# Kernel optimization log

Hardware: AMD Instinct MI355X
Metric: run time of the kernel (lower is better)

## Reference

```python
import jax, jax.numpy as jnp
import numpy as np

N_NODES = 50000
BN_EPS = 1e-5


def graph_conv(x, row, col, ew, n):
    # deg from source indices only (matches torch.bincount(row))
    deg = jnp.zeros((n,), x.dtype).at[row].add(1.0)
    dinv = jnp.where(deg > 0, deg ** -0.5, 0.0)
    norm = dinv[row] * ew * dinv[col]                     # [E]
    msg = norm[:, None] * x[row]                          # [E, F]
    return jax.ops.segment_sum(msg, col, num_segments=n)  # out[dst] += w * x[src]


def batch_norm(x, gamma, beta):
    # training-mode BN over the node (batch) dim, biased variance
    mu = jnp.mean(x, axis=0)
    var = jnp.mean((x - mu) ** 2, axis=0)
    return (x - mu) / jnp.sqrt(var + BN_EPS) * gamma + beta


def setup_inputs() -> dict:
    key = jax.random.key(0)
    ks = jax.random.split(key, 12)
    node_features = jax.random.normal(ks[0], (N_NODES, 100), dtype=jnp.float32)
    edge_index = jax.random.randint(ks[1], (2, 800000), 0, N_NODES, dtype=jnp.int64)
    edge_weights = jax.random.uniform(ks[2], (800000,), dtype=jnp.float32)
    def lin(k, fi, fo):
        lim = 1.0 / np.sqrt(fi)
        k1, k2 = jax.random.split(k)
        W = jax.random.uniform(k1, (fi, fo), minval=-lim, maxval=lim, dtype=jnp.float32)
        b = jax.random.uniform(k2, (fo,), minval=-lim, maxval=lim, dtype=jnp.float32)
        return W, b
    W0, b0 = lin(ks[3], 100, 128)
    W1, b1 = lin(ks[4], 128, 128)
    W2, b2 = lin(ks[5], 128, 64)
    return {
        "node_features": node_features, "edge_index": edge_index, "edge_weights": edge_weights,
        "W0": W0, "b0": b0, "g0": jnp.ones((128,), jnp.float32), "be0": jnp.zeros((128,), jnp.float32),
        "W1": W1, "b1": b1, "g1": jnp.ones((128,), jnp.float32), "be1": jnp.zeros((128,), jnp.float32),
        "W2": W2, "b2": b2,
    }


def reference(node_features, edge_index, edge_weights,
              W0, b0, g0, be0, W1, b1, g1, be1, W2, b2):
    n = node_features.shape[0]
    row, col = edge_index[0], edge_index[1]
    x = node_features
    # layer 0
    x = graph_conv(x, row, col, edge_weights, n)
    x = jax.nn.relu(batch_norm(x @ W0 + b0, g0, be0))
    # layer 1
    x = graph_conv(x, row, col, edge_weights, n)
    x = jax.nn.relu(batch_norm(x @ W1 + b1, g1, be1))
    # final layer (no BN/relu)
    x = graph_conv(x, row, col, edge_weights, n)
    return x @ W2 + b2
```

## Files before the change

### kernel.cpp

```cpp
#include <hip/hip_runtime.h>
#include <cstdint>

#define F0 100
#define FH 128
#define FO 64
#define BN_EPS 1e-5f

typedef unsigned short ushort_t;
typedef unsigned int uint_t;

static inline int ceil_div(long long a, long long b) { return (int)((a + b - 1) / b); }

__device__ __forceinline__ float bf_lo(uint_t w) { return __uint_as_float(w << 16); }
__device__ __forceinline__ float bf_hi(uint_t w) { return __uint_as_float(w & 0xffff0000u); }
__device__ __forceinline__ uint_t f2bf(float f) {
  uint_t u = __float_as_uint(f);
  return (u + 0x7fffu + ((u >> 16) & 1u)) >> 16;
}
__device__ __forceinline__ uint_t pack2(float a, float b) {
  return f2bf(a) | (f2bf(b) << 16);
}


template <int K, int F, int TM, bool BN_A, bool A_BF16, bool OUT_BF16>
__device__ __forceinline__ void gemm2_body(int bid, const void* __restrict__ A_,
                                           const float* __restrict__ W,
                                           const float* __restrict__ bias,
                                           const float* __restrict__ scA,
                                           const float* __restrict__ shA,
                                           void* __restrict__ out_, int n) {
  constexpr int NCG = F / 4;
  constexpr int NRG = 256 / NCG;
  constexpr int BR = NRG * TM;
  constexpr int BK = 32;
  constexpr int F4 = F / 4;

  __shared__ float sW[BK][F];
  __shared__ float sA[BR][BK];

  const int tid = threadIdx.x;
  const int cg = tid % NCG;
  const int rg = tid / NCG;
  const int row0 = bid * BR;

  float4 acc[TM];
#pragma unroll
  for (int t = 0; t < TM; ++t) acc[t] = make_float4(0.f, 0.f, 0.f, 0.f);

  const float4* W4 = (const float4*)W;
  const float4 z4 = make_float4(0.f, 0.f, 0.f, 0.f);

  for (int k0 = 0; k0 < K; k0 += BK) {
    for (int i = tid; i < BK * F4; i += 256) {
      int kk = i / F4, f4 = i % F4;
      int gk = k0 + kk;
      ((float4*)&sW[kk][0])[f4] = (gk < K) ? W4[(size_t)gk * F4 + f4] : z4;
    }
    for (int i = tid; i < BR * (BK / 4); i += 256) {
      int r = i / (BK / 4), k4 = i % (BK / 4);
      int gr = row0 + r;
      int gk = k0 + k4 * 4;
      float4 av = z4;
      if (gr < n && gk + 3 < K) {
        if (A_BF16) {
          uint2 u = ((const uint2*)A_)[(size_t)gr * (K / 4) + (gk >> 2)];
          av.x = bf_lo(u.x); av.y = bf_hi(u.x);
          av.z = bf_lo(u.y); av.w = bf_hi(u.y);
        } else {
          av = ((const float4*)A_)[(size_t)gr * (K / 4) + (gk >> 2)];
        }
        if (BN_A) {
          float4 sc = ((const float4*)scA)[gk >> 2];
          float4 sh = ((const float4*)shA)[gk >> 2];
          av.x = fmaxf(fmaf(av.x, sc.x, sh.x), 0.f);
          av.y = fmaxf(fmaf(av.y, sc.y, sh.y), 0.f);
          av.z = fmaxf(fmaf(av.z, sc.z, sh.z), 0.f);
          av.w = fmaxf(fmaf(av.w, sc.w, sh.w), 0.f);
        }
      }
      ((float4*)&sA[r][0])[k4] = av;
    }
    __syncthreads();
#pragma unroll 4
    for (int kk = 0; kk < BK; ++kk) {
      float4 w = ((const float4*)&sW[kk][0])[cg];
#pragma unroll
      for (int t = 0; t < TM; ++t) {
        float a = sA[rg * TM + t][kk];
        acc[t].x = fmaf(a, w.x, acc[t].x);
        acc[t].y = fmaf(a, w.y, acc[t].y);
        acc[t].z = fmaf(a, w.z, acc[t].z);
        acc[t].w = fmaf(a, w.w, acc[t].w);
      }
    }
    __syncthreads();
  }

  float4 bb = bias ? ((const float4*)bias)[cg] : z4;
#pragma unroll
  for (int t = 0; t < TM; ++t) {
    int gr = row0 + rg * TM + t;
    if (gr < n) {
      float4 v = acc[t];
      v.x += bb.x; v.y += bb.y; v.z += bb.z; v.w += bb.w;
      if (OUT_BF16) {
        ((uint2*)out_)[(size_t)gr * F4 + cg] = make_uint2(pack2(v.x, v.y), pack2(v.z, v.w));
      } else {
        ((float4*)out_)[(size_t)gr * F4 + cg] = v;
      }
    }
  }
}

template <int K, int F, int TM, bool BN_A, bool A_BF16, bool OUT_BF16>
__global__ __launch_bounds__(256) void gemm2_kernel(const void* __restrict__ A,
                                                    const float* __restrict__ W,
                                                    const float* __restrict__ bias,
                                                    const float* __restrict__ scA,
                                                    const float* __restrict__ shA,
                                                    void* __restrict__ out, int n) {
  gemm2_body<K, F, TM, BN_A, A_BF16, OUT_BF16>(blockIdx.x, A, W, bias, scA, shA, out, n);
}


__global__ __launch_bounds__(256) void fused_gemm_hist_kernel(
    const float* __restrict__ A, const float* __restrict__ W, void* __restrict__ out, int n,
    int GB, const int* __restrict__ row, const int* __restrict__ col,
    int* __restrict__ degr, int* __restrict__ degc, int* __restrict__ posw, int E) {
  int bid = blockIdx.x;
  int r5 = bid % 5;
  int g = bid / 5;
  if (r5 == 0 && g < GB) {
    gemm2_body<F0, FH, 8, false, false, true>(g, A, W, nullptr, nullptr, nullptr, out, n);
    return;
  }
  int h = (r5 == 0) ? (bid - GB) : (bid - (g + 1));
  int e = h * 256 + threadIdx.x;
  if (e >= E) return;
  int r = row[e], c = col[e];
  atomicAdd(&degr[r], 1);
  int pos = atomicAdd(&degc[c], 1);
  posw[e] = pos;
}


__global__ __launch_bounds__(256) void scan_fused_kernel(const int* __restrict__ degr,
                                                         const int* __restrict__ degc,
                                                         float* __restrict__ dinv,
                                                         int* __restrict__ startA,
                                                         int* __restrict__ bsums, int n) {
  __shared__ int s[256];
  int i = blockIdx.x * 256 + threadIdx.x;
  int dc = 0;
  if (i < n) {
    int dr = degr[i];
    dc = degc[i];
    dinv[i] = (dr > 0) ? rsqrtf((float)dr) : 0.0f;
  }
  s[threadIdx.x] = dc;
  __syncthreads();
  for (int off = 1; off < 256; off <<= 1) {
    int t = 0;
    if (threadIdx.x >= off) t = s[threadIdx.x - off];
    __syncthreads();
    if (threadIdx.x >= off) s[threadIdx.x] += t;
    __syncthreads();
  }
  if (i < n) startA[i] = s[threadIdx.x] - dc;
  if (threadIdx.x == 255) bsums[blockIdx.x] = s[255];
}

__global__ __launch_bounds__(256) void scan_partials_kernel(int* __restrict__ bsums, int nb) {
  __shared__ int s[256];
  int v = (threadIdx.x < nb) ? bsums[threadIdx.x] : 0;
  s[threadIdx.x] = v;
  __syncthreads();
  for (int off = 1; off < 256; off <<= 1) {
    int t = 0;
    if (threadIdx.x >= off) t = s[threadIdx.x - off];
    __syncthreads();
    if (threadIdx.x >= off) s[threadIdx.x] += t;
    __syncthreads();
  }
  if (threadIdx.x < nb) bsums[threadIdx.x] = s[threadIdx.x] - v;
}

__global__ __launch_bounds__(256) void scan_add_kernel(int* __restrict__ startA,
                                                       const int* __restrict__ bsums, int n) {
  int i = blockIdx.x * 256 + threadIdx.x;
  if (i < n) startA[i] += bsums[blockIdx.x];
}


__global__ __launch_bounds__(256) void csr_scatter2_kernel(const int* __restrict__ row,
                                                           const int* __restrict__ col,
                                                           const float* __restrict__ ew,
                                                           const float* __restrict__ dinv,
                                                           const int* __restrict__ startA,
                                                           const int* __restrict__ posw,
                                                           int2* __restrict__ ep, int E) {
  int e = blockIdx.x * blockDim.x + threadIdx.x;
  if (e >= E) return;
  int r = row[e], c = col[e];
  int pos = startA[c] + posw[e];
  float coef = dinv[r] * ew[e] * dinv[c];
  ep[pos] = make_int2(r, __float_as_int(coef));
}


template <int F, bool DO_BN, bool OUT_F32>
__global__ __launch_bounds__(256) void conv_bf16_kernel(const ushort_t* __restrict__ x,
                                                        const int* __restrict__ startA,
                                                        const int* __restrict__ degc,
                                                        const int2* __restrict__ ep,
                                                        const float* __restrict__ bias,
                                                        const float* __restrict__ scale,
                                                        const float* __restrict__ shift,
                                                        void* __restrict__ out, int n) {
  constexpr int G2 = F / 8;
  constexpr int TPD = G2 / 2;
  long long tid = (long long)blockIdx.x * 256 + threadIdx.x;
  if (tid >= (long long)n * TPD) return;
  int dst = (int)(tid / TPD);
  int q = (int)(tid % TPD);
  int s0 = startA[dst];
  int d = degc[dst];
  const uint4* x4 = (const uint4*)x;

  float sc[16], sh[16];
  if (DO_BN) {
#pragma unroll
    for (int ch = 0; ch < 2; ++ch) {
      int g = q + ch * TPD;
#pragma unroll
      for (int j = 0; j < 8; ++j) {
        sc[ch * 8 + j] = scale[g * 8 + j];
        sh[ch * 8 + j] = shift[g * 8 + j];
      }
    }
  }

  float acc[16];
#pragma unroll
  for (int j = 0; j < 16; ++j) acc[j] = 0.f;

  for (int k = 0; k < d; ++k) {
    int2 e = ep[s0 + k];
    float c = __int_as_float(e.y);
    const uint4* xp = x4 + (size_t)e.x * G2 + q;
    uint4 v0 = xp[0];
    uint4 v1 = xp[TPD];
    uint_t vv[8] = {v0.x, v0.y, v0.z, v0.w, v1.x, v1.y, v1.z, v1.w};
#pragma unroll
    for (int h = 0; h < 8; ++h) {
      float f0 = bf_lo(vv[h]);
      float f1 = bf_hi(vv[h]);
      if (DO_BN) {
        f0 = fmaxf(fmaf(f0, sc[2 * h], sh[2 * h]), 0.f);
        f1 = fmaxf(fmaf(f1, sc[2 * h + 1], sh[2 * h + 1]), 0.f);
      }
      acc[2 * h] = fmaf(c, f0, acc[2 * h]);
      acc[2 * h + 1] = fmaf(c, f1, acc[2 * h + 1]);
    }
  }

  if (bias) {
#pragma unroll
    for (int ch = 0; ch < 2; ++ch) {
      int g = q + ch * TPD;
#pragma unroll
      for (int j = 0; j < 8; ++j) acc[ch * 8 + j] += bias[g * 8 + j];
    }
  }

  if (OUT_F32) {
    float4* o4 = (float4*)out;
    size_t base = (size_t)dst * (F / 4);
    o4[base + 2 * q] = make_float4(acc[0], acc[1], acc[2], acc[3]);
    o4[base + 2 * q + 1] = make_float4(acc[4], acc[5], acc[6], acc[7]);
    o4[base + 2 * (q + TPD)] = make_float4(acc[8], acc[9], acc[10], acc[11]);
    o4[base + 2 * (q + TPD) + 1] = make_float4(acc[12], acc[13], acc[14], acc[15]);
  } else {
    uint4* o4 = (uint4*)out;
    size_t base = (size_t)dst * G2;
    o4[base + q] = make_uint4(pack2(acc[0], acc[1]), pack2(acc[2], acc[3]),
                              pack2(acc[4], acc[5]), pack2(acc[6], acc[7]));
    o4[base + q + TPD] = make_uint4(pack2(acc[8], acc[9]), pack2(acc[10], acc[11]),
                                    pack2(acc[12], acc[13]), pack2(acc[14], acc[15]));
  }
}


__global__ __launch_bounds__(128) void bn_stats_bf16_kernel(const ushort_t* __restrict__ z,
                                                            float* __restrict__ sum,
                                                            float* __restrict__ sumsq, int n) {
  int f = threadIdx.x;
  float s = 0.0f, s2 = 0.0f;
  for (int r = blockIdx.x; r < n; r += gridDim.x) {
    float v = __uint_as_float(((uint_t)z[(size_t)r * FH + f]) << 16);
    s += v;
    s2 += v * v;
  }
  unsafeAtomicAdd(&sum[f], s);
  unsafeAtomicAdd(&sumsq[f], s2);
}

__global__ __launch_bounds__(128) void bn_finalize_kernel(const float* __restrict__ sum,
                                                          const float* __restrict__ sumsq,
                                                          const float* __restrict__ g,
                                                          const float* __restrict__ be,
                                                          float* __restrict__ scale,
                                                          float* __restrict__ shift, int n) {
  int f = threadIdx.x;
  float invN = 1.0f / (float)n;
  float mean = sum[f] * invN;
  float var = sumsq[f] * invN - mean * mean;
  var = fmaxf(var, 0.0f);
  float sc = g[f] / sqrtf(var + BN_EPS);
  scale[f] = sc;
  shift[f] = be[f] - mean * sc;
}


extern "C" void kernel_launch(void* const* d_in, const int* in_sizes, int n_in,
                              void* d_out, int out_size, void* d_ws, size_t ws_size,
                              hipStream_t stream) {
  const float* x   = (const float*)d_in[0];
  const int*   ei  = (const int*)d_in[1];
  const float* ew  = (const float*)d_in[2];
  const float* W0  = (const float*)d_in[3];
  const float* b0  = (const float*)d_in[4];
  const float* g0  = (const float*)d_in[5];
  const float* be0 = (const float*)d_in[6];
  const float* W1  = (const float*)d_in[7];
  const float* b1  = (const float*)d_in[8];
  const float* g1  = (const float*)d_in[9];
  const float* be1 = (const float*)d_in[10];
  const float* W2  = (const float*)d_in[11];
  const float* b2  = (const float*)d_in[12];

  const int n = in_sizes[0] / F0;
  const int E = in_sizes[2];
  const int* row = ei;
  const int* col = ei + E;

  ushort_t* bufA  = (ushort_t*)d_ws;
  ushort_t* bufB  = bufA + (size_t)n * FH;
  int2*   ep      = (int2*)(bufB + (size_t)n * FH);
  int*    degc    = (int*)(ep + E);
  int*    degr    = degc + n;
  int*    startA  = degr + n;
  float*  dinv    = (float*)(startA + n);
  int*    bsums   = (int*)(dinv + n);
  float*  sum0    = (float*)(bsums + 256);
  float*  sumsq0  = sum0 + FH;
  float*  sum1    = sumsq0 + FH;
  float*  sumsq1  = sum1 + FH;
  float*  scale0  = sumsq1 + FH;
  float*  shift0  = scale0 + FH;
  float*  scale1  = shift0 + FH;
  float*  shift1  = scale1 + FH;
  int*    posw    = (int*)bufB;

  const int nb = ceil_div(n, 256);
  const int GB = ceil_div(n, 64);
  const int HB = ceil_div(E, 256);
  const int CB_H = ceil_div((long long)n * (FH / 16), 256);
  const int CB_O = ceil_div((long long)n * (FO / 16), 256);

  (void)hipMemsetAsync(degc, 0, 2 * (size_t)n * sizeof(int), stream);
  (void)hipMemsetAsync(sum0, 0, 4 * FH * sizeof(float), stream);
  fused_gemm_hist_kernel<<<GB + HB, 256, 0, stream>>>(x, W0, bufA, n, GB, row, col,
                                                      degr, degc, posw, E);
  scan_fused_kernel<<<nb, 256, 0, stream>>>(degr, degc, dinv, startA, bsums, n);
  scan_partials_kernel<<<1, 256, 0, stream>>>(bsums, nb);
  scan_add_kernel<<<nb, 256, 0, stream>>>(startA, bsums, n);
  csr_scatter2_kernel<<<HB, 256, 0, stream>>>(row, col, ew, dinv, startA, posw, ep, E);

  conv_bf16_kernel<FH, false, false><<<CB_H, 256, 0, stream>>>(
      bufA, startA, degc, ep, b0, nullptr, nullptr, bufB, n);
  bn_stats_bf16_kernel<<<256, 128, 0, stream>>>(bufB, sum0, sumsq0, n);
  bn_finalize_kernel<<<1, 128, 0, stream>>>(sum0, sumsq0, g0, be0, scale0, shift0, n);

  conv_bf16_kernel<FH, true, false><<<CB_H, 256, 0, stream>>>(
      bufB, startA, degc, ep, nullptr, scale0, shift0, bufA, n);
  gemm2_kernel<FH, FH, 8, false, true, true><<<GB, 256, 0, stream>>>(
      bufA, W1, b1, nullptr, nullptr, bufB, n);
  bn_stats_bf16_kernel<<<256, 128, 0, stream>>>(bufB, sum1, sumsq1, n);
  bn_finalize_kernel<<<1, 128, 0, stream>>>(sum1, sumsq1, g1, be1, scale1, shift1, n);

  gemm2_kernel<FH, FO, 4, true, true, true><<<GB, 256, 0, stream>>>(
      bufB, W2, nullptr, scale1, shift1, bufA, n);
  conv_bf16_kernel<FO, false, true><<<CB_O, 256, 0, stream>>>(
      bufA, startA, degc, ep, b2, nullptr, nullptr, (float*)d_out, n);
}
```

Measured before the change: 390.8 us.

## Fuse scan offsets into consumers, stage edges in LDS, merge BN finalize

Drops the scan_add kernel: consumers add block partial sums to local prefix offsets on the fly. The first GEMM now runs alongside the CSR scatter instead of the histogram, and the separate BN finalize kernels fold into the stats kernels through a last-block counter. The conv kernels cooperatively load each block's contiguous edge range into shared memory in chunks before gathering. This cuts launches and makes edge-list reads coalesced, at the cost of extra barriers and an extra offset lookup.

Result: slower. 406.2 us (+3.9%).

```diff
diff --git a/kernel.cpp b/kernel.cpp
--- a/kernel.cpp
+++ b/kernel.cpp
@@ -123,31 +123,22 @@
 }
 
 
-__global__ __launch_bounds__(256) void fused_gemm_hist_kernel(
-    const float* __restrict__ A, const float* __restrict__ W, void* __restrict__ out, int n,
-    int GB, const int* __restrict__ row, const int* __restrict__ col,
-    int* __restrict__ degr, int* __restrict__ degc, int* __restrict__ posw, int E) {
-  int bid = blockIdx.x;
-  int r5 = bid % 5;
-  int g = bid / 5;
-  if (r5 == 0 && g < GB) {
-    gemm2_body<F0, FH, 8, false, false, true>(g, A, W, nullptr, nullptr, nullptr, out, n);
-    return;
-  }
-  int h = (r5 == 0) ? (bid - GB) : (bid - (g + 1));
-  int e = h * 256 + threadIdx.x;
+__global__ __launch_bounds__(256) void hist_pos_kernel(const int* __restrict__ row,
+                                                       const int* __restrict__ col,
+                                                       int* __restrict__ degr,
+                                                       int* __restrict__ degc,
+                                                       int* __restrict__ posw, int E) {
+  int e = blockIdx.x * blockDim.x + threadIdx.x;
   if (e >= E) return;
-  int r = row[e], c = col[e];
-  atomicAdd(&degr[r], 1);
-  int pos = atomicAdd(&degc[c], 1);
-  posw[e] = pos;
+  atomicAdd(&degr[row[e]], 1);
+  posw[e] = atomicAdd(&degc[col[e]], 1);
 }
 
 
 __global__ __launch_bounds__(256) void scan_fused_kernel(const int* __restrict__ degr,
                                                          const int* __restrict__ degc,
                                                          float* __restrict__ dinv,
-                                                         int* __restrict__ startA,
+                                                         int* __restrict__ startp,
                                                          int* __restrict__ bsums, int n) {
   __shared__ int s[256];
   int i = blockIdx.x * 256 + threadIdx.x;
@@ -166,7 +157,7 @@
     if (threadIdx.x >= off) s[threadIdx.x] += t;
     __syncthreads();
   }
-  if (i < n) startA[i] = s[threadIdx.x] - dc;
+  if (i < n) startp[i] = s[threadIdx.x] - dc;
   if (threadIdx.x == 255) bsums[blockIdx.x] = s[255];
 }
 
@@ -185,24 +176,25 @@
   if (threadIdx.x < nb) bsums[threadIdx.x] = s[threadIdx.x] - v;
 }
 
-__global__ __launch_bounds__(256) void scan_add_kernel(int* __restrict__ startA,
-                                                       const int* __restrict__ bsums, int n) {
-  int i = blockIdx.x * 256 + threadIdx.x;
-  if (i < n) startA[i] += bsums[blockIdx.x];
-}
-
-
-__global__ __launch_bounds__(256) void csr_scatter2_kernel(const int* __restrict__ row,
-                                                           const int* __restrict__ col,
-                                                           const float* __restrict__ ew,
-                                                           const float* __restrict__ dinv,
-                                                           const int* __restrict__ startA,
-                                                           const int* __restrict__ posw,
-                                                           int2* __restrict__ ep, int E) {
-  int e = blockIdx.x * blockDim.x + threadIdx.x;
+
+__global__ __launch_bounds__(256) void fused_scatter_gemm_kernel(
+    const int* __restrict__ row, const int* __restrict__ col, const float* __restrict__ ew,
+    const float* __restrict__ dinv, const int* __restrict__ startp,
+    const int* __restrict__ bsums, const int* __restrict__ posw, int2* __restrict__ ep, int E,
+    const float* __restrict__ A, const float* __restrict__ W, void* __restrict__ out, int n,
+    int GB) {
+  int bid = blockIdx.x;
+  int r5 = bid % 5;
+  int g = bid / 5;
+  if (r5 == 0 && g < GB) {
+    gemm2_body<F0, FH, 8, false, false, true>(g, A, W, nullptr, nullptr, nullptr, out, n);
+    return;
+  }
+  int h = (r5 == 0) ? (bid - GB) : (bid - (g + 1));
+  int e = h * 256 + threadIdx.x;
   if (e >= E) return;
   int r = row[e], c = col[e];
-  int pos = startA[c] + posw[e];
+  int pos = startp[c] + bsums[c >> 8] + posw[e];
   float coef = dinv[r] * ew[e] * dinv[c];
   ep[pos] = make_int2(r, __float_as_int(coef));
 }
@@ -210,21 +202,35 @@
 
 template <int F, bool DO_BN, bool OUT_F32>
 __global__ __launch_bounds__(256) void conv_bf16_kernel(const ushort_t* __restrict__ x,
-                                                        const int* __restrict__ startA,
+                                                        const int* __restrict__ startp,
+                                                        const int* __restrict__ bsums,
                                                         const int* __restrict__ degc,
                                                         const int2* __restrict__ ep,
                                                         const float* __restrict__ bias,
                                                         const float* __restrict__ scale,
                                                         const float* __restrict__ shift,
-                                                        void* __restrict__ out, int n) {
+                                                        void* __restrict__ out, int n, int E) {
   constexpr int G2 = F / 8;
   constexpr int TPD = G2 / 2;
-  long long tid = (long long)blockIdx.x * 256 + threadIdx.x;
-  if (tid >= (long long)n * TPD) return;
-  int dst = (int)(tid / TPD);
-  int q = (int)(tid % TPD);
-  int s0 = startA[dst];
-  int d = degc[dst];
+  constexpr int DPB = 256 / TPD;
+  constexpr int CHUNK = 1024;
+  __shared__ int2 eps[CHUNK];
+
+  const int d0 = blockIdx.x * DPB;
+  const int dst = d0 + threadIdx.x / TPD;
+  const int q = threadIdx.x % TPD;
+  const bool valid = dst < n;
+
+  const int blkStart = startp[d0] + bsums[d0 >> 8];
+  const int dEnd0 = (d0 + DPB < n) ? (d0 + DPB) : n;
+  const int blkEnd = (dEnd0 < n) ? (startp[dEnd0] + bsums[dEnd0 >> 8]) : E;
+
+  int s0 = 0, myEnd = 0;
+  if (valid) {
+    s0 = startp[dst] + bsums[dst >> 8];
+    myEnd = s0 + degc[dst];
+  }
+
   const uint4* x4 = (const uint4*)x;
 
   float sc[16], sh[16];
@@ -244,25 +250,37 @@
 #pragma unroll
   for (int j = 0; j < 16; ++j) acc[j] = 0.f;
 
-  for (int k = 0; k < d; ++k) {
-    int2 e = ep[s0 + k];
-    float c = __int_as_float(e.y);
-    const uint4* xp = x4 + (size_t)e.x * G2 + q;
-    uint4 v0 = xp[0];
-    uint4 v1 = xp[TPD];
-    uint_t vv[8] = {v0.x, v0.y, v0.z, v0.w, v1.x, v1.y, v1.z, v1.w};
-#pragma unroll
-    for (int h = 0; h < 8; ++h) {
-      float f0 = bf_lo(vv[h]);
-      float f1 = bf_hi(vv[h]);
-      if (DO_BN) {
-        f0 = fmaxf(fmaf(f0, sc[2 * h], sh[2 * h]), 0.f);
-        f1 = fmaxf(fmaf(f1, sc[2 * h + 1], sh[2 * h + 1]), 0.f);
+  for (int cb = blkStart; cb < blkEnd; cb += CHUNK) {
+    int cnt = min(CHUNK, blkEnd - cb);
+    if (cb != blkStart) __syncthreads();
+    for (int i = threadIdx.x; i < cnt; i += 256) eps[i] = ep[cb + i];
+    __syncthreads();
+    if (valid) {
+      int k0 = max(s0, cb);
+      int k1 = min(myEnd, cb + cnt);
+      for (int k = k0; k < k1; ++k) {
+        int2 e = eps[k - cb];
+        float c = __int_as_float(e.y);
+        const uint4* xp = x4 + (size_t)e.x * G2 + q;
+        uint4 v0 = xp[0];
+        uint4 v1 = xp[TPD];
+        uint_t vv[8] = {v0.x, v0.y, v0.z, v0.w, v1.x, v1.y, v1.z, v1.w};
+#pragma unroll
+        for (int hh = 0; hh < 8; ++hh) {
+          float f0 = bf_lo(vv[hh]);
+          float f1 = bf_hi(vv[hh]);
+          if (DO_BN) {
+            f0 = fmaxf(fmaf(f0, sc[2 * hh], sh[2 * hh]), 0.f);
+            f1 = fmaxf(fmaf(f1, sc[2 * hh + 1], sh[2 * hh + 1]), 0.f);
+          }
+          acc[2 * hh] = fmaf(c, f0, acc[2 * hh]);
+          acc[2 * hh + 1] = fmaf(c, f1, acc[2 * hh + 1]);
+        }
       }
-      acc[2 * h] = fmaf(c, f0, acc[2 * h]);
-      acc[2 * h + 1] = fmaf(c, f1, acc[2 * h + 1]);
-    }
-  }
+    }
+  }
+
+  if (!valid) return;
 
   if (bias) {
 #pragma unroll
@@ -291,9 +309,14 @@
 }
 
 
-__global__ __launch_bounds__(128) void bn_stats_bf16_kernel(const ushort_t* __restrict__ z,
-                                                            float* __restrict__ sum,
-                                                            float* __restrict__ sumsq, int n) {
+__global__ __launch_bounds__(128) void bn_stats_fin_kernel(const ushort_t* __restrict__ z,
+                                                           float* __restrict__ sum,
+                                                           float* __restrict__ sumsq,
+                                                           const float* __restrict__ g,
+                                                           const float* __restrict__ be,
+                                                           float* __restrict__ scale,
+                                                           float* __restrict__ shift,
+                                                           int n, int* __restrict__ ctr) {
   int f = threadIdx.x;
   float s = 0.0f, s2 = 0.0f;
   for (int r = blockIdx.x; r < n; r += gridDim.x) {
@@ -303,22 +326,21 @@
   }
   unsafeAtomicAdd(&sum[f], s);
   unsafeAtomicAdd(&sumsq[f], s2);
-}
-
-__global__ __launch_bounds__(128) void bn_finalize_kernel(const float* __restrict__ sum,
-                                                          const float* __restrict__ sumsq,
-                                                          const float* __restrict__ g,
-                                                          const float* __restrict__ be,
-                                                          float* __restrict__ scale,
-                                                          float* __restrict__ shift, int n) {
-  int f = threadIdx.x;
-  float invN = 1.0f / (float)n;
-  float mean = sum[f] * invN;
-  float var = sumsq[f] * invN - mean * mean;
-  var = fmaxf(var, 0.0f);
-  float sc = g[f] / sqrtf(var + BN_EPS);
-  scale[f] = sc;
-  shift[f] = be[f] - mean * sc;
+  __threadfence();
+  __syncthreads();
+  __shared__ int lastFlag;
+  if (f == 0) lastFlag = (atomicAdd(ctr, 1) == (int)gridDim.x - 1) ? 1 : 0;
+  __syncthreads();
+  if (lastFlag) {
+    float S = atomicAdd(&sum[f], 0.0f);
+    float S2 = atomicAdd(&sumsq[f], 0.0f);
+    float invN = 1.0f / (float)n;
+    float mean = S * invN;
+    float var = fmaxf(S2 * invN - mean * mean, 0.0f);
+    float sc = g[f] / sqrtf(var + BN_EPS);
+    scale[f] = sc;
+    shift[f] = be[f] - mean * sc;
+  }
 }
 
 
@@ -349,14 +371,16 @@
   int2*   ep      = (int2*)(bufB + (size_t)n * FH);
   int*    degc    = (int*)(ep + E);
   int*    degr    = degc + n;
-  int*    startA  = degr + n;
-  float*  dinv    = (float*)(startA + n);
-  int*    bsums   = (int*)(dinv + n);
-  float*  sum0    = (float*)(bsums + 256);
+  float*  sum0    = (float*)(degr + n);
   float*  sumsq0  = sum0 + FH;
   float*  sum1    = sumsq0 + FH;
   float*  sumsq1  = sum1 + FH;
-  float*  scale0  = sumsq1 + FH;
+  int*    ctr     = (int*)(sumsq1 + FH);
+  const size_t zero_bytes = (2 * (size_t)n + 4 * FH + 2) * 4;
+  int*    startp  = ctr + 2;
+  float*  dinv    = (float*)(startp + n);
+  int*    bsums   = (int*)(dinv + n);
+  float*  scale0  = (float*)(bsums + 256);
   float*  shift0  = scale0 + FH;
   float*  scale1  = shift0 + FH;
   float*  shift1  = scale1 + FH;
@@ -365,32 +389,30 @@
   const int nb = ceil_div(n, 256);
   const int GB = ceil_div(n, 64);
   const int HB = ceil_div(E, 256);
-  const int CB_H = ceil_div((long long)n * (FH / 16), 256);
-  const int CB_O = ceil_div((long long)n * (FO / 16), 256);
-
-  (void)hipMemsetAsync(degc, 0, 2 * (size_t)n * sizeof(int), stream);
-  (void)hipMemsetAsync(sum0, 0, 4 * FH * sizeof(float), stream);
-  fused_gemm_hist_kernel<<<GB + HB, 256, 0, stream>>>(x, W0, bufA, n, GB, row, col,
-                                                      degr, degc, posw, E);
-  scan_fused_kernel<<<nb, 256, 0, stream>>>(degr, degc, dinv, startA, bsums, n);
+  const int CB_H = ceil_div(n, 32);
+  const int CB_O = ceil_div(n, 64);
+
+  (void)hipMemsetAsync(degc, 0, zero_bytes, stream);
+  hist_pos_kernel<<<HB, 256, 0, stream>>>(row, col, degr, degc, posw, E);
+  scan_fused_kernel<<<nb, 256, 0, stream>>>(degr, degc, dinv, startp, bsums, n);
   scan_partials_kernel<<<1, 256, 0, stream>>>(bsums, nb);
-  scan_add_kernel<<<nb, 256, 0, stream>>>(startA, bsums, n);
-  csr_scatter2_kernel<<<HB, 256, 0, stream>>>(row, col, ew, dinv, startA, posw, ep, E);
+  fused_scatter_gemm_kernel<<<GB + HB, 256, 0, stream>>>(row, col, ew, dinv, startp, bsums,
+                                                         posw, ep, E, x, W0, bufA, n, GB);
 
   conv_bf16_kernel<FH, false, false><<<CB_H, 256, 0, stream>>>(
-      bufA, startA, degc, ep, b0, nullptr, nullptr, bufB, n);
-  bn_stats_bf16_kernel<<<256, 128, 0, stream>>>(bufB, sum0, sumsq0, n);
-  bn_finalize_kernel<<<1, 128, 0, stream>>>(sum0, sumsq0, g0, be0, scale0, shift0, n);
+      bufA, startp, bsums, degc, ep, b0, nullptr, nullptr, bufB, n, E);
+  bn_stats_fin_kernel<<<256, 128, 0, stream>>>(bufB, sum0, sumsq0, g0, be0, scale0, shift0,
+                                               n, ctr + 0);
 
   conv_bf16_kernel<FH, true, false><<<CB_H, 256, 0, stream>>>(
-      bufB, startA, degc, ep, nullptr, scale0, shift0, bufA, n);
+      bufB, startp, bsums, degc, ep, nullptr, scale0, shift0, bufA, n, E);
   gemm2_kernel<FH, FH, 8, false, true, true><<<GB, 256, 0, stream>>>(
       bufA, W1, b1, nullptr, nullptr, bufB, n);
-  bn_stats_bf16_kernel<<<256, 128, 0, stream>>>(bufB, sum1, sumsq1, n);
-  bn_finalize_kernel<<<1, 128, 0, stream>>>(sum1, sumsq1, g1, be1, scale1, shift1, n);
+  bn_stats_fin_kernel<<<256, 128, 0, stream>>>(bufB, sum1, sumsq1, g1, be1, scale1, shift1,
+                                               n, ctr + 1);
 
   gemm2_kernel<FH, FO, 4, true, true, true><<<GB, 256, 0, stream>>>(
       bufB, W2, nullptr, scale1, shift1, bufA, n);
   conv_bf16_kernel<FO, false, true><<<CB_O, 256, 0, stream>>>(
-      bufA, startA, degc, ep, b2, nullptr, nullptr, (float*)d_out, n);
-}
+      bufA, startp, bsums, degc, ep, b2, nullptr, nullptr, (float*)d_out, n, E);
+}
```
